# Kernel tuning notes

Measured on AMD Instinct MI355X. Metric: run time of the kernel, lower is better.

Reference implementation:

```python
import jax, jax.numpy as jnp
import numpy as np

B, L, D, H = 2, 1024, 1024, 16
HD = D // H  # 64


def _skew(x):
    # x: (BH, L, 2L-1) -> (BH, L, L); Music-Transformer skew trick.
    BH, Lx, _ = x.shape
    x = jnp.pad(x, ((0, 0), (0, 0), (1, 0)))            # (BH, L, 2L)
    x = x.reshape(BH, 2 * Lx * Lx)                        # flatten
    x = jnp.pad(x, ((0, 0), (0, Lx - 1)))                 # append L-1 zeros
    x = x.reshape(BH, Lx + 1, 2 * Lx - 1)
    return x[:, :Lx, Lx - 1:]


def setup_inputs() -> dict:
    key = jax.random.key(0)
    ks = jax.random.split(key, 10)
    s = 1.0 / np.sqrt(D)
    return {
        "x": jax.random.normal(ks[0], (B, L, D), jnp.float32),
        "Wq": jax.random.normal(ks[1], (D, D), jnp.float32) * s,
        "bq": jnp.zeros((D,), jnp.float32),
        "Wk": jax.random.normal(ks[2], (D, D), jnp.float32) * s,
        "bk": jnp.zeros((D,), jnp.float32),
        "Wv": jax.random.normal(ks[3], (D, D), jnp.float32) * s,
        "bv": jnp.zeros((D,), jnp.float32),
        "Wo": jax.random.normal(ks[4], (D, D), jnp.float32) * s,
        "bo": jnp.zeros((D,), jnp.float32),
        "rel_pos_emb": jax.random.normal(ks[5], (2 * L - 1, HD), jnp.float32),
    }


def reference(x, Wq, bq, Wk, bk, Wv, bv, Wo, bo, rel_pos_emb):
    Bx, Lx, Dx = x.shape
    hd = Dx // H
    scale = hd ** (-0.5)
    # projections (torch Linear: x @ W.T + b)
    q = (x @ Wq.T + bq).reshape(Bx, Lx, H, hd).transpose(0, 2, 1, 3)  # (B,H,L,hd)
    k = (x @ Wk.T + bk).reshape(Bx, Lx, H, hd).transpose(0, 2, 1, 3)
    v = (x @ Wv.T + bv).reshape(Bx, Lx, H, hd).transpose(0, 2, 1, 3)
    scores = jnp.einsum('bhid,bhjd->bhij', q, k)                      # (B,H,L,L)
    rel = jnp.einsum('bhid,rd->bhir', q, rel_pos_emb)                 # (B,H,L,2L-1)
    rel = _skew(rel.reshape(Bx * H, Lx, 2 * Lx - 1)).reshape(Bx, H, Lx, Lx)
    attn = jax.nn.softmax((scores + rel) * scale, axis=-1)
    ctx = jnp.einsum('bhij,bhjd->bhid', attn, v)                      # (B,H,L,hd)
    ctx = ctx.transpose(0, 2, 1, 3).reshape(Bx, Lx, Dx)
    return ctx @ Wo.T + bo
```

## Files before the change

### kernel.cpp

```cpp
#include <hip/hip_runtime.h>
#include <hip/hip_bf16.h>

typedef __bf16 bf16_t;
typedef __bf16 bf16x8 __attribute__((ext_vector_type(8)));
typedef __bf16 bf16x4 __attribute__((ext_vector_type(4)));
typedef float f32x4 __attribute__((ext_vector_type(4)));

#define B_ 2
#define L_ 1024
#define D_ 1024
#define H_ 16
#define HD_ 64

template <int CTRL>
static __device__ __forceinline__ float dpp_fmax(float v) {
    const int t = __builtin_amdgcn_update_dpp(0, __float_as_int(v), CTRL,
                                              0xF, 0xF, true);
    return fmaxf(v, __int_as_float(t));
}

__global__ __launch_bounds__(256) void prep_kernel(
    const float* __restrict__ x,
    const float* __restrict__ Wq, const float* __restrict__ Wk,
    const float* __restrict__ Wv, const float* __restrict__ Wo,
    const float* __restrict__ E,
    bf16_t* __restrict__ xb,
    bf16_t* __restrict__ Wqb, bf16_t* __restrict__ Wkb,
    bf16_t* __restrict__ Wvb, bf16_t* __restrict__ Wob,
    bf16_t* __restrict__ Eb) {
    const int bid = blockIdx.x;
    if (bid < 6144) {
        const float* src;
        bf16_t* dst;
        int i;
        if (bid < 2048) {
            src = x; dst = xb; i = bid * 256 + threadIdx.x;
        } else {
            const int z = (bid - 2048) >> 10;
            src = (z == 0) ? Wq : (z == 1) ? Wk : (z == 2) ? Wv : Wo;
            dst = (z == 0) ? Wqb : (z == 1) ? Wkb : (z == 2) ? Wvb : Wob;
            i = ((bid - 2048) & 1023) * 256 + threadIdx.x;
        }
        const float4 v = ((const float4*)src)[i];
        bf16x4 o;
        o[0] = (bf16_t)v.x; o[1] = (bf16_t)v.y;
        o[2] = (bf16_t)v.z; o[3] = (bf16_t)v.w;
        ((bf16x4*)dst)[i] = o;
    } else {
        const int idx = (bid - 6144) * 256 + threadIdx.x;
        if (idx < 64) Eb[idx] = (bf16_t)0.f;
        if (idx < 2047 * 64) Eb[64 + idx] = (bf16_t)E[idx];
    }
}

__global__ __launch_bounds__(256) void qkv_gemm_kernel(
    const bf16_t* __restrict__ xb,
    const bf16_t* __restrict__ Wqb, const bf16_t* __restrict__ Wkb,
    const bf16_t* __restrict__ Wvb,
    const float* __restrict__ bq, const float* __restrict__ bk2,
    const float* __restrict__ bv2,
    bf16_t* __restrict__ qbh, bf16_t* __restrict__ kbh,
    bf16_t* __restrict__ vtb) {
    constexpr int K = D_;
    __shared__ __align__(16) bf16_t As[64][72];
    __shared__ __align__(16) bf16_t Bs[64][72];

    const int z = blockIdx.z;
    const bf16_t* W = (z == 0) ? Wqb : (z == 1) ? Wkb : Wvb;
    const float* bias = (z == 0) ? bq : (z == 1) ? bk2 : bv2;
    const float alpha = (z == 0) ? 0.125f : 1.0f;

    const int tid = threadIdx.x;
    const int m0 = blockIdx.y * 64;
    const int n0 = blockIdx.x * 64;
    const int wave = tid >> 6;
    const int lane = tid & 63;
    const int wm = (wave >> 1) << 5;
    const int wn = (wave & 1) << 5;
    const int lrow = lane & 15;
    const int quad = lane >> 4;
    const int r0 = tid >> 3;
    const int c8 = (tid & 7) << 3;

    f32x4 acc[2][2] = {};

    uint4 pA0 = *(const uint4*)&xb[(size_t)(m0 + r0) * K + c8];
    uint4 pA1 = *(const uint4*)&xb[(size_t)(m0 + r0 + 32) * K + c8];
    uint4 pB0 = *(const uint4*)&W[(size_t)(n0 + r0) * K + c8];
    uint4 pB1 = *(const uint4*)&W[(size_t)(n0 + r0 + 32) * K + c8];

    for (int k0 = 0; k0 < K; k0 += 64) {
        *(uint4*)&As[r0][c8] = pA0;
        *(uint4*)&As[r0 + 32][c8] = pA1;
        *(uint4*)&Bs[r0][c8] = pB0;
        *(uint4*)&Bs[r0 + 32][c8] = pB1;
        const int kn = (k0 + 64 < K) ? k0 + 64 : k0;
        pA0 = *(const uint4*)&xb[(size_t)(m0 + r0) * K + kn + c8];
        pA1 = *(const uint4*)&xb[(size_t)(m0 + r0 + 32) * K + kn + c8];
        pB0 = *(const uint4*)&W[(size_t)(n0 + r0) * K + kn + c8];
        pB1 = *(const uint4*)&W[(size_t)(n0 + r0 + 32) * K + kn + c8];
        __syncthreads();

#pragma unroll
        for (int kc = 0; kc < 2; ++kc) {
            bf16x8 af[2], bfr[2];
            af[0]  = *(const bf16x8*)&As[wm + lrow][kc * 32 + 8 * quad];
            af[1]  = *(const bf16x8*)&As[wm + 16 + lrow][kc * 32 + 8 * quad];
            bfr[0] = *(const bf16x8*)&Bs[wn + lrow][kc * 32 + 8 * quad];
            bfr[1] = *(const bf16x8*)&Bs[wn + 16 + lrow][kc * 32 + 8 * quad];
#pragma unroll
            for (int t = 0; t < 2; ++t)
#pragma unroll
                for (int u = 0; u < 2; ++u)
                    acc[t][u] = __builtin_amdgcn_mfma_f32_16x16x32_bf16(
                        af[t], bfr[u], acc[t][u], 0, 0, 0);
        }
        __syncthreads();
    }

#pragma unroll
    for (int t = 0; t < 2; ++t) {
#pragma unroll
        for (int u = 0; u < 2; ++u) {
            const int col = n0 + wn + u * 16 + lrow;
            const float bvv = bias[col];
            const int h = col >> 6, d = col & 63;
            if (z < 2) {
                bf16_t* outp = z ? kbh : qbh;
#pragma unroll
                for (int r = 0; r < 4; ++r) {
                    const int row = m0 + wm + t * 16 + quad * 4 + r;
                    const int b = row >> 10, i = row & 1023;
                    outp[((size_t)((b * H_ + h) * L_ + i)) * HD_ + d] =
                        (bf16_t)((acc[t][u][r] + bvv) * alpha);
                }
            } else {
                const int row0 = m0 + wm + t * 16 + quad * 4;
                const int b = row0 >> 10, i = row0 & 1023;
                bf16x4 pk;
#pragma unroll
                for (int r = 0; r < 4; ++r) pk[r] = (bf16_t)(acc[t][u][r] + bvv);
                *(bf16x4*)&vtb[((size_t)((b * H_ + h) * HD_ + d)) * L_ + i] = pk;
            }
        }
    }
}

__global__ __launch_bounds__(256) void out_gemm_kernel(
    const bf16_t* __restrict__ A, const bf16_t* __restrict__ W,
    const float* __restrict__ bias, float* __restrict__ outF) {
    constexpr int K = D_;
    __shared__ __align__(16) bf16_t As[64][72];
    __shared__ __align__(16) bf16_t Bs[64][72];

    const int tid = threadIdx.x;
    const int m0 = blockIdx.y * 64;
    const int n0 = blockIdx.x * 64;
    const int wave = tid >> 6;
    const int lane = tid & 63;
    const int wm = (wave >> 1) << 5;
    const int wn = (wave & 1) << 5;
    const int lrow = lane & 15;
    const int quad = lane >> 4;
    const int r0 = tid >> 3;
    const int c8 = (tid & 7) << 3;

    f32x4 acc[2][2] = {};

    uint4 pA0 = *(const uint4*)&A[(size_t)(m0 + r0) * K + c8];
    uint4 pA1 = *(const uint4*)&A[(size_t)(m0 + r0 + 32) * K + c8];
    uint4 pB0 = *(const uint4*)&W[(size_t)(n0 + r0) * K + c8];
    uint4 pB1 = *(const uint4*)&W[(size_t)(n0 + r0 + 32) * K + c8];

    for (int k0 = 0; k0 < K; k0 += 64) {
        *(uint4*)&As[r0][c8] = pA0;
        *(uint4*)&As[r0 + 32][c8] = pA1;
        *(uint4*)&Bs[r0][c8] = pB0;
        *(uint4*)&Bs[r0 + 32][c8] = pB1;
        const int kn = (k0 + 64 < K) ? k0 + 64 : k0;
        pA0 = *(const uint4*)&A[(size_t)(m0 + r0) * K + kn + c8];
        pA1 = *(const uint4*)&A[(size_t)(m0 + r0 + 32) * K + kn + c8];
        pB0 = *(const uint4*)&W[(size_t)(n0 + r0) * K + kn + c8];
        pB1 = *(const uint4*)&W[(size_t)(n0 + r0 + 32) * K + kn + c8];
        __syncthreads();

#pragma unroll
        for (int kc = 0; kc < 2; ++kc) {
            bf16x8 af[2], bfr[2];
            af[0]  = *(const bf16x8*)&As[wm + lrow][kc * 32 + 8 * quad];
            af[1]  = *(const bf16x8*)&As[wm + 16 + lrow][kc * 32 + 8 * quad];
            bfr[0] = *(const bf16x8*)&Bs[wn + lrow][kc * 32 + 8 * quad];
            bfr[1] = *(const bf16x8*)&Bs[wn + 16 + lrow][kc * 32 + 8 * quad];
#pragma unroll
            for (int t = 0; t < 2; ++t)
#pragma unroll
                for (int u = 0; u < 2; ++u)
                    acc[t][u] = __builtin_amdgcn_mfma_f32_16x16x32_bf16(
                        af[t], bfr[u], acc[t][u], 0, 0, 0);
        }
        __syncthreads();
    }

#pragma unroll
    for (int t = 0; t < 2; ++t) {
#pragma unroll
        for (int u = 0; u < 2; ++u) {
            const int col = n0 + wn + u * 16 + lrow;
            const float bvv = bias[col];
#pragma unroll
            for (int r = 0; r < 4; ++r) {
                const int row = m0 + wm + t * 16 + quad * 4 + r;
                outF[(size_t)row * D_ + col] = acc[t][u][r] + bvv;
            }
        }
    }
}

__global__ __launch_bounds__(256) void fattn_kernel(
    const bf16_t* __restrict__ qbh, const bf16_t* __restrict__ kbh,
    const bf16_t* __restrict__ vtb, const bf16_t* __restrict__ Eb,
    bf16_t* __restrict__ ctx) {
    __shared__ __align__(16) char smem[33792];
    float (*Om)[32][64] = (float(*)[32][64])smem;
    float (*ml)[32][2]  = (float(*)[32][2])(smem + 32768);

    const int tid = threadIdx.x;
    const int w = tid >> 6;
    const int lane = tid & 63;
    const int q4 = lane >> 4;
    const int n = lane & 15;
    const int bh = blockIdx.y;
    const int b = bh >> 4;
    const int h = bh & 15;
    const int ib = blockIdx.x * 32;

    bf16_t* band = (bf16_t*)smem + (size_t)w * (96 * 40);
    bf16_t* ps = band;

    bf16x8 ones;
#pragma unroll
    for (int e = 0; e < 8; ++e) ones[e] = (bf16_t)1.0f;

    bf16x8 aq[2][2];
#pragma unroll
    for (int m = 0; m < 2; ++m) {
        const bf16x8* qrow =
            (const bf16x8*)(qbh + ((size_t)bh * L_ + ib + 16 * m + n) * HD_);
        aq[m][0] = qrow[q4];
        aq[m][1] = qrow[4 + q4];
    }

    const bf16_t* vbase = vtb + (size_t)bh * HD_ * L_;

    f32x4 o[2][4] = {};
    float m_r[2][4], l_r[2][4];
#pragma unroll
    for (int m = 0; m < 2; ++m)
#pragma unroll
        for (int r = 0; r < 4; ++r) { m_r[m][r] = -1e30f; l_r[m][r] = 0.f; }

    for (int t = 0; t < 4; ++t) {
        const int j0 = w * 256 + t * 64;

        bf16x8 bk[4][2];
#pragma unroll
        for (int u = 0; u < 4; ++u)
#pragma unroll
            for (int kc = 0; kc < 2; ++kc)
                bk[u][kc] = *(const bf16x8*)(kbh +
                    ((size_t)bh * L_ + j0 + 16 * u + n) * HD_ + kc * 32 + 8 * q4);

        const int rbase = j0 - ib + 992;
#pragma unroll
        for (int up = 0; up < 6; ++up) {
            f32x4 rc[2] = {};
#pragma unroll
            for (int kc = 0; kc < 2; ++kc) {
                const bf16x8 be = *(const bf16x8*)(Eb +
                    ((size_t)(rbase + 16 * up + n)) * HD_ + kc * 32 + 8 * q4);
#pragma unroll
                for (int m = 0; m < 2; ++m)
                    rc[m] = __builtin_amdgcn_mfma_f32_16x16x32_bf16(
                        aq[m][kc], be, rc[m], 0, 0, 0);
            }
#pragma unroll
            for (int m = 0; m < 2; ++m) {
                bf16x4 pk;
#pragma unroll
                for (int r = 0; r < 4; ++r) pk[r] = (bf16_t)rc[m][r];
                *(bf16x4*)&band[(size_t)(16 * up + n) * 40 + 16 * m + 4 * q4] = pk;
            }
        }

        f32x4 s[2][4] = {};
#pragma unroll
        for (int u = 0; u < 4; ++u)
#pragma unroll
            for (int kc = 0; kc < 2; ++kc)
#pragma unroll
                for (int m = 0; m < 2; ++m)
                    s[m][u] = __builtin_amdgcn_mfma_f32_16x16x32_bf16(
                        aq[m][kc], bk[u][kc], s[m][u], 0, 0, 0);

        bf16x8 vf[4][2];
#pragma unroll
        for (int u = 0; u < 4; ++u)
#pragma unroll
            for (int kc = 0; kc < 2; ++kc)
                vf[u][kc] = *(const bf16x8*)(vbase +
                    ((size_t)(16 * u + n)) * L_ + j0 + kc * 32 + 8 * q4);

#pragma unroll
        for (int m = 0; m < 2; ++m)
#pragma unroll
            for (int u = 0; u < 4; ++u)
#pragma unroll
                for (int r = 0; r < 4; ++r) {
                    const int row = 16 * m + 4 * q4 + r;
                    s[m][u][r] +=
                        (float)band[(size_t)(16 * u + n - row + 31) * 40 + row];
                }

        float al[2][4];
#pragma unroll
        for (int m = 0; m < 2; ++m) {
#pragma unroll
            for (int r = 0; r < 4; ++r) {
                float mt = fmaxf(fmaxf(s[m][0][r], s[m][1][r]),
                                 fmaxf(s[m][2][r], s[m][3][r]));
                mt = dpp_fmax<0x121>(mt);
                mt = dpp_fmax<0x122>(mt);
                mt = dpp_fmax<0x124>(mt);
                mt = dpp_fmax<0x128>(mt);
                const float mn = fmaxf(m_r[m][r], mt);
                al[m][r] = __expf(m_r[m][r] - mn);
                m_r[m][r] = mn;
#pragma unroll
                for (int u = 0; u < 4; ++u) {
                    s[m][u][r] = __expf(s[m][u][r] - mn);
                    o[m][u][r] *= al[m][r];
                }
            }
        }

#pragma unroll
        for (int m = 0; m < 2; ++m)
#pragma unroll
            for (int u = 0; u < 4; ++u)
#pragma unroll
                for (int r = 0; r < 4; ++r)
                    ps[(size_t)(16 * m + 4 * q4 + r) * 72 + 16 * u + n] =
                        (bf16_t)s[m][u][r];

        bf16x8 pa[2][2];
#pragma unroll
        for (int m = 0; m < 2; ++m) {
            pa[m][0] = *(const bf16x8*)&ps[(size_t)(16 * m + n) * 72 + 8 * q4];
            pa[m][1] = *(const bf16x8*)&ps[(size_t)(16 * m + n) * 72 + 32 + 8 * q4];
        }

#pragma unroll
        for (int m = 0; m < 2; ++m) {
            f32x4 z = {};
            z = __builtin_amdgcn_mfma_f32_16x16x32_bf16(pa[m][0], ones, z, 0, 0, 0);
            z = __builtin_amdgcn_mfma_f32_16x16x32_bf16(pa[m][1], ones, z, 0, 0, 0);
#pragma unroll
            for (int r = 0; r < 4; ++r)
                l_r[m][r] = l_r[m][r] * al[m][r] + z[r];
        }

#pragma unroll
        for (int u = 0; u < 4; ++u)
#pragma unroll
            for (int kc = 0; kc < 2; ++kc)
#pragma unroll
                for (int m = 0; m < 2; ++m)
                    o[m][u] = __builtin_amdgcn_mfma_f32_16x16x32_bf16(
                        pa[m][kc], vf[u][kc], o[m][u], 0, 0, 0);
    }

    __syncthreads();
#pragma unroll
    for (int m = 0; m < 2; ++m)
#pragma unroll
        for (int u = 0; u < 4; ++u)
#pragma unroll
            for (int r = 0; r < 4; ++r)
                Om[w][16 * m + 4 * q4 + r][16 * u + n] = o[m][u][r];
    if (n == 0) {
#pragma unroll
        for (int m = 0; m < 2; ++m)
#pragma unroll
            for (int r = 0; r < 4; ++r) {
                ml[w][16 * m + 4 * q4 + r][0] = m_r[m][r];
                ml[w][16 * m + 4 * q4 + r][1] = l_r[m][r];
            }
    }
    __syncthreads();

    {
        const int row = tid >> 3;
        const int c0 = (tid & 7) * 8;
        const float m0v = ml[0][row][0], m1v = ml[1][row][0];
        const float m2v = ml[2][row][0], m3v = ml[3][row][0];
        const float ms = fmaxf(fmaxf(m0v, m1v), fmaxf(m2v, m3v));
        const float a0 = __expf(m0v - ms), a1 = __expf(m1v - ms);
        const float a2 = __expf(m2v - ms), a3 = __expf(m3v - ms);
        const float inv = 1.f / (a0 * ml[0][row][1] + a1 * ml[1][row][1] +
                                 a2 * ml[2][row][1] + a3 * ml[3][row][1]);
        bf16_t* dst = ctx + ((size_t)(b * L_ + ib + row)) * D_ + h * HD_ + c0;
#pragma unroll
        for (int cc = 0; cc < 8; ++cc) {
            const int col = c0 + cc;
            const float val = (a0 * Om[0][row][col] + a1 * Om[1][row][col] +
                               a2 * Om[2][row][col] + a3 * Om[3][row][col]) * inv;
            dst[cc] = (bf16_t)val;
        }
    }
}

extern "C" void kernel_launch(void* const* d_in, const int* in_sizes, int n_in,
                              void* d_out, int out_size, void* d_ws,
                              size_t ws_size, hipStream_t stream) {
    const float* x   = (const float*)d_in[0];
    const float* Wq  = (const float*)d_in[1];
    const float* bq  = (const float*)d_in[2];
    const float* Wk  = (const float*)d_in[3];
    const float* bk  = (const float*)d_in[4];
    const float* Wv  = (const float*)d_in[5];
    const float* bv  = (const float*)d_in[6];
    const float* Wo  = (const float*)d_in[7];
    const float* bo  = (const float*)d_in[8];
    const float* E   = (const float*)d_in[9];
    float* out = (float*)d_out;

    char* ws = (char*)d_ws;
    const size_t MB = 1024u * 1024u;
    bf16_t* xb   = (bf16_t*)(ws);
    bf16_t* Wqb  = (bf16_t*)(ws + 4 * MB);
    bf16_t* Wkb  = (bf16_t*)(ws + 6 * MB);
    bf16_t* Wvb  = (bf16_t*)(ws + 8 * MB);
    bf16_t* Wob  = (bf16_t*)(ws + 10 * MB);
    bf16_t* qbh  = (bf16_t*)(ws + 12 * MB);
    bf16_t* kbh  = (bf16_t*)(ws + 16 * MB);
    bf16_t* vtb  = (bf16_t*)(ws + 20 * MB);
    bf16_t* ctxb = (bf16_t*)(ws + 24 * MB);
    bf16_t* Eb   = (bf16_t*)(ws + 28 * MB);

    prep_kernel<<<6656, 256, 0, stream>>>(x, Wq, Wk, Wv, Wo, E,
                                          xb, Wqb, Wkb, Wvb, Wob, Eb);

    dim3 gq(D_ / 64, (B_ * L_) / 64, 3);
    qkv_gemm_kernel<<<gq, 256, 0, stream>>>(xb, Wqb, Wkb, Wvb, bq, bk, bv,
                                            qbh, kbh, vtb);

    dim3 ga(L_ / 32, B_ * H_);
    fattn_kernel<<<ga, 256, 0, stream>>>(qbh, kbh, vtb, Eb, ctxb);

    dim3 gg(D_ / 64, (B_ * L_) / 64);
    out_gemm_kernel<<<gg, 256, 0, stream>>>(ctxb, Wob, bo, out);
}
```

Before: 185.0 us.

## Halve attention query tile to 16 rows, use exp2 softmax, vectorize ctx store

The attention kernel now handles 16 query rows per block instead of 32, doubling the grid to 64x32 blocks, shrinking shared memory, and adding a launch-bounds occupancy hint of 5. The q scale folds in log2(e) so softmax can use the native exp2 instruction instead of __expf. The final context write packs four bf16 values into one vector store, and the Om buffer is padded to 65 columns to avoid bank conflicts. Smaller tiles mean K/V/E fragments are reloaded twice as often per query row, which trades data reuse for occupancy and parallelism.

Measured after the change: 237.9 us. +28.6%, slower.

```diff
diff --git a/kernel.cpp b/kernel.cpp
--- a/kernel.cpp
+++ b/kernel.cpp
@@ -68,7 +68,7 @@
     const int z = blockIdx.z;
     const bf16_t* W = (z == 0) ? Wqb : (z == 1) ? Wkb : Wvb;
     const float* bias = (z == 0) ? bq : (z == 1) ? bk2 : bv2;
-    const float alpha = (z == 0) ? 0.125f : 1.0f;
+    const float alpha = (z == 0) ? 0.18033688011112043f : 1.0f;
 
     const int tid = threadIdx.x;
     const int m0 = blockIdx.y * 64;
@@ -216,13 +216,13 @@
     }
 }
 
-__global__ __launch_bounds__(256) void fattn_kernel(
+__global__ __launch_bounds__(256, 5) void fattn_kernel(
     const bf16_t* __restrict__ qbh, const bf16_t* __restrict__ kbh,
     const bf16_t* __restrict__ vtb, const bf16_t* __restrict__ Eb,
     bf16_t* __restrict__ ctx) {
-    __shared__ __align__(16) char smem[33792];
-    float (*Om)[32][64] = (float(*)[32][64])smem;
-    float (*ml)[32][2]  = (float(*)[32][2])(smem + 32768);
+    __shared__ __align__(16) char smem[25600];
+    float (*Om)[16][65] = (float(*)[16][65])smem;
+    float (*ml)[16][2]  = (float(*)[16][2])(smem + 16640);
 
     const int tid = threadIdx.x;
     const int w = tid >> 6;
@@ -232,32 +232,29 @@
     const int bh = blockIdx.y;
     const int b = bh >> 4;
     const int h = bh & 15;
-    const int ib = blockIdx.x * 32;
-
-    bf16_t* band = (bf16_t*)smem + (size_t)w * (96 * 40);
+    const int ib = blockIdx.x * 16;
+
+    bf16_t* band = (bf16_t*)smem + (size_t)w * (80 * 40);
     bf16_t* ps = band;
 
     bf16x8 ones;
 #pragma unroll
     for (int e = 0; e < 8; ++e) ones[e] = (bf16_t)1.0f;
 
-    bf16x8 aq[2][2];
-#pragma unroll
-    for (int m = 0; m < 2; ++m) {
+    bf16x8 aq[2];
+    {
         const bf16x8* qrow =
-            (const bf16x8*)(qbh + ((size_t)bh * L_ + ib + 16 * m + n) * HD_);
-        aq[m][0] = qrow[q4];
-        aq[m][1] = qrow[4 + q4];
+            (const bf16x8*)(qbh + ((size_t)bh * L_ + ib + n) * HD_);
+        aq[0] = qrow[q4];
+        aq[1] = qrow[4 + q4];
     }
 
     const bf16_t* vbase = vtb + (size_t)bh * HD_ * L_;
 
-    f32x4 o[2][4] = {};
-    float m_r[2][4], l_r[2][4];
-#pragma unroll
-    for (int m = 0; m < 2; ++m)
-#pragma unroll
-        for (int r = 0; r < 4; ++r) { m_r[m][r] = -1e30f; l_r[m][r] = 0.f; }
+    f32x4 o[4] = {};
+    float m_r[4], l_r[4];
+#pragma unroll
+    for (int r = 0; r < 4; ++r) { m_r[r] = -1e30f; l_r[r] = 0.f; }
 
     for (int t = 0; t < 4; ++t) {
         const int j0 = w * 256 + t * 64;
@@ -270,37 +267,30 @@
                 bk[u][kc] = *(const bf16x8*)(kbh +
                     ((size_t)bh * L_ + j0 + 16 * u + n) * HD_ + kc * 32 + 8 * q4);
 
-        const int rbase = j0 - ib + 992;
-#pragma unroll
-        for (int up = 0; up < 6; ++up) {
-            f32x4 rc[2] = {};
+        const int rbase = j0 - ib + 1008;
+#pragma unroll
+        for (int up = 0; up < 5; ++up) {
+            f32x4 rc = {};
 #pragma unroll
             for (int kc = 0; kc < 2; ++kc) {
                 const bf16x8 be = *(const bf16x8*)(Eb +
                     ((size_t)(rbase + 16 * up + n)) * HD_ + kc * 32 + 8 * q4);
-#pragma unroll
-                for (int m = 0; m < 2; ++m)
-                    rc[m] = __builtin_amdgcn_mfma_f32_16x16x32_bf16(
-                        aq[m][kc], be, rc[m], 0, 0, 0);
+                rc = __builtin_amdgcn_mfma_f32_16x16x32_bf16(
+                    aq[kc], be, rc, 0, 0, 0);
             }
-#pragma unroll
-            for (int m = 0; m < 2; ++m) {
-                bf16x4 pk;
-#pragma unroll
-                for (int r = 0; r < 4; ++r) pk[r] = (bf16_t)rc[m][r];
-                *(bf16x4*)&band[(size_t)(16 * up + n) * 40 + 16 * m + 4 * q4] = pk;
-            }
-        }
-
-        f32x4 s[2][4] = {};
+            bf16x4 pk;
+#pragma unroll
+            for (int r = 0; r < 4; ++r) pk[r] = (bf16_t)rc[r];
+            *(bf16x4*)&band[(size_t)(16 * up + n) * 40 + 4 * q4] = pk;
+        }
+
+        f32x4 s[4] = {};
 #pragma unroll
         for (int u = 0; u < 4; ++u)
 #pragma unroll
             for (int kc = 0; kc < 2; ++kc)
-#pragma unroll
-                for (int m = 0; m < 2; ++m)
-                    s[m][u] = __builtin_amdgcn_mfma_f32_16x16x32_bf16(
-                        aq[m][kc], bk[u][kc], s[m][u], 0, 0, 0);
+                s[u] = __builtin_amdgcn_mfma_f32_16x16x32_bf16(
+                    aq[kc], bk[u][kc], s[u], 0, 0, 0);
 
         bf16x8 vf[4][2];
 #pragma unroll
@@ -311,111 +301,97 @@
                     ((size_t)(16 * u + n)) * L_ + j0 + kc * 32 + 8 * q4);
 
 #pragma unroll
-        for (int m = 0; m < 2; ++m)
-#pragma unroll
-            for (int u = 0; u < 4; ++u)
-#pragma unroll
-                for (int r = 0; r < 4; ++r) {
-                    const int row = 16 * m + 4 * q4 + r;
-                    s[m][u][r] +=
-                        (float)band[(size_t)(16 * u + n - row + 31) * 40 + row];
-                }
-
-        float al[2][4];
-#pragma unroll
-        for (int m = 0; m < 2; ++m) {
+        for (int u = 0; u < 4; ++u)
 #pragma unroll
             for (int r = 0; r < 4; ++r) {
-                float mt = fmaxf(fmaxf(s[m][0][r], s[m][1][r]),
-                                 fmaxf(s[m][2][r], s[m][3][r]));
-                mt = dpp_fmax<0x121>(mt);
-                mt = dpp_fmax<0x122>(mt);
-                mt = dpp_fmax<0x124>(mt);
-                mt = dpp_fmax<0x128>(mt);
-                const float mn = fmaxf(m_r[m][r], mt);
-                al[m][r] = __expf(m_r[m][r] - mn);
-                m_r[m][r] = mn;
-#pragma unroll
-                for (int u = 0; u < 4; ++u) {
-                    s[m][u][r] = __expf(s[m][u][r] - mn);
-                    o[m][u][r] *= al[m][r];
-                }
+                const int row = 4 * q4 + r;
+                s[u][r] +=
+                    (float)band[(size_t)(16 * u + n - row + 15) * 40 + row];
             }
-        }
-
-#pragma unroll
-        for (int m = 0; m < 2; ++m)
-#pragma unroll
-            for (int u = 0; u < 4; ++u)
-#pragma unroll
-                for (int r = 0; r < 4; ++r)
-                    ps[(size_t)(16 * m + 4 * q4 + r) * 72 + 16 * u + n] =
-                        (bf16_t)s[m][u][r];
-
-        bf16x8 pa[2][2];
-#pragma unroll
-        for (int m = 0; m < 2; ++m) {
-            pa[m][0] = *(const bf16x8*)&ps[(size_t)(16 * m + n) * 72 + 8 * q4];
-            pa[m][1] = *(const bf16x8*)&ps[(size_t)(16 * m + n) * 72 + 32 + 8 * q4];
-        }
-
-#pragma unroll
-        for (int m = 0; m < 2; ++m) {
+
+        float al[4];
+#pragma unroll
+        for (int r = 0; r < 4; ++r) {
+            float mt = fmaxf(fmaxf(s[0][r], s[1][r]),
+                             fmaxf(s[2][r], s[3][r]));
+            mt = dpp_fmax<0x121>(mt);
+            mt = dpp_fmax<0x122>(mt);
+            mt = dpp_fmax<0x124>(mt);
+            mt = dpp_fmax<0x128>(mt);
+            const float mn = fmaxf(m_r[r], mt);
+            al[r] = __builtin_amdgcn_exp2f(m_r[r] - mn);
+            m_r[r] = mn;
+#pragma unroll
+            for (int u = 0; u < 4; ++u) {
+                s[u][r] = __builtin_amdgcn_exp2f(s[u][r] - mn);
+                o[u][r] *= al[r];
+            }
+        }
+
+#pragma unroll
+        for (int u = 0; u < 4; ++u)
+#pragma unroll
+            for (int r = 0; r < 4; ++r)
+                ps[(size_t)(4 * q4 + r) * 72 + 16 * u + n] = (bf16_t)s[u][r];
+
+        bf16x8 pa[2];
+        pa[0] = *(const bf16x8*)&ps[(size_t)n * 72 + 8 * q4];
+        pa[1] = *(const bf16x8*)&ps[(size_t)n * 72 + 32 + 8 * q4];
+
+        {
             f32x4 z = {};
-            z = __builtin_amdgcn_mfma_f32_16x16x32_bf16(pa[m][0], ones, z, 0, 0, 0);
-            z = __builtin_amdgcn_mfma_f32_16x16x32_bf16(pa[m][1], ones, z, 0, 0, 0);
+            z = __builtin_amdgcn_mfma_f32_16x16x32_bf16(pa[0], ones, z, 0, 0, 0);
+            z = __builtin_amdgcn_mfma_f32_16x16x32_bf16(pa[1], ones, z, 0, 0, 0);
 #pragma unroll
             for (int r = 0; r < 4; ++r)
-                l_r[m][r] = l_r[m][r] * al[m][r] + z[r];
+                l_r[r] = l_r[r] * al[r] + z[r];
         }
 
 #pragma unroll
         for (int u = 0; u < 4; ++u)
 #pragma unroll
             for (int kc = 0; kc < 2; ++kc)
-#pragma unroll
-                for (int m = 0; m < 2; ++m)
-                    o[m][u] = __builtin_amdgcn_mfma_f32_16x16x32_bf16(
-                        pa[m][kc], vf[u][kc], o[m][u], 0, 0, 0);
+                o[u] = __builtin_amdgcn_mfma_f32_16x16x32_bf16(
+                    pa[kc], vf[u][kc], o[u], 0, 0, 0);
     }
 
     __syncthreads();
 #pragma unroll
-    for (int m = 0; m < 2; ++m)
-#pragma unroll
-        for (int u = 0; u < 4; ++u)
-#pragma unroll
-            for (int r = 0; r < 4; ++r)
-                Om[w][16 * m + 4 * q4 + r][16 * u + n] = o[m][u][r];
+    for (int u = 0; u < 4; ++u)
+#pragma unroll
+        for (int r = 0; r < 4; ++r)
+            Om[w][4 * q4 + r][16 * u + n] = o[u][r];
     if (n == 0) {
 #pragma unroll
-        for (int m = 0; m < 2; ++m)
-#pragma unroll
-            for (int r = 0; r < 4; ++r) {
-                ml[w][16 * m + 4 * q4 + r][0] = m_r[m][r];
-                ml[w][16 * m + 4 * q4 + r][1] = l_r[m][r];
-            }
+        for (int r = 0; r < 4; ++r) {
+            ml[w][4 * q4 + r][0] = m_r[r];
+            ml[w][4 * q4 + r][1] = l_r[r];
+        }
     }
     __syncthreads();
 
     {
-        const int row = tid >> 3;
-        const int c0 = (tid & 7) * 8;
+        const int row = tid >> 4;
+        const int c0 = (tid & 15) * 4;
         const float m0v = ml[0][row][0], m1v = ml[1][row][0];
         const float m2v = ml[2][row][0], m3v = ml[3][row][0];
         const float ms = fmaxf(fmaxf(m0v, m1v), fmaxf(m2v, m3v));
-        const float a0 = __expf(m0v - ms), a1 = __expf(m1v - ms);
-        const float a2 = __expf(m2v - ms), a3 = __expf(m3v - ms);
+        const float a0 = __builtin_amdgcn_exp2f(m0v - ms);
+        const float a1 = __builtin_amdgcn_exp2f(m1v - ms);
+        const float a2 = __builtin_amdgcn_exp2f(m2v - ms);
+        const float a3 = __builtin_amdgcn_exp2f(m3v - ms);
         const float inv = 1.f / (a0 * ml[0][row][1] + a1 * ml[1][row][1] +
                                  a2 * ml[2][row][1] + a3 * ml[3][row][1]);
         bf16_t* dst = ctx + ((size_t)(b * L_ + ib + row)) * D_ + h * HD_ + c0;
-#pragma unroll
-        for (int cc = 0; cc < 8; ++cc) {
+        bf16x4 pk;
+#pragma unroll
+        for (int cc = 0; cc < 4; ++cc) {
             const int col = c0 + cc;
             const float val = (a0 * Om[0][row][col] + a1 * Om[1][row][col] +
                                a2 * Om[2][row][col] + a3 * Om[3][row][col]) * inv;
-            dst[cc] = (bf16_t)val;
-        }
+            pk[cc] = (bf16_t)val;
+        }
+        *(bf16x4*)dst = pk;
     }
 }
 
@@ -454,7 +430,7 @@
     qkv_gemm_kernel<<<gq, 256, 0, stream>>>(xb, Wqb, Wkb, Wvb, bq, bk, bv,
                                             qbh, kbh, vtb);
 
-    dim3 ga(L_ / 32, B_ * H_);
+    dim3 ga(L_ / 16, B_ * H_);
     fattn_kernel<<<ga, 256, 0, stream>>>(qbh, kbh, vtb, Eb, ctxb);
 
     dim3 gg(D_ / 64, (B_ * L_) / 64);
```

## Use 128x128 GEMM tiles with direct global-to-LDS loads and exp2 softmax

Applied to the files above, without the earlier changes.

Both projection GEMMs move from 64x64 to 128x128 block tiles, with each wave computing a 64x64 sub-tile. They now fill shared memory with global_load_lds direct-to-LDS transfers instead of register prefetch followed by LDS stores. The attention softmax switches from __expf to the hardware exp2 instruction, with log2(e) folded into the Q scaling constant. This cuts global traffic per FLOP and exp overhead, but the grids become small (128 blocks for the output GEMM). The unpadded LDS rows may also cause bank conflicts, and the prefetch overlap between loads and MFMA is lost.

New measurement: 198.2 us. 7.1% more time.

```diff
diff --git a/kernel.cpp b/kernel.cpp
--- a/kernel.cpp
+++ b/kernel.cpp
@@ -11,6 +11,9 @@
 #define D_ 1024
 #define H_ 16
 #define HD_ 64
+
+#define AS1 __attribute__((address_space(1)))
+#define AS3 __attribute__((address_space(3)))
 
 template <int CTRL>
 static __device__ __forceinline__ float dpp_fmax(float v) {
@@ -62,56 +65,57 @@
     bf16_t* __restrict__ qbh, bf16_t* __restrict__ kbh,
     bf16_t* __restrict__ vtb) {
     constexpr int K = D_;
-    __shared__ __align__(16) bf16_t As[64][72];
-    __shared__ __align__(16) bf16_t Bs[64][72];
+    __shared__ __align__(16) bf16_t As[128 * 64];
+    __shared__ __align__(16) bf16_t Bs[128 * 64];
 
     const int z = blockIdx.z;
     const bf16_t* W = (z == 0) ? Wqb : (z == 1) ? Wkb : Wvb;
     const float* bias = (z == 0) ? bq : (z == 1) ? bk2 : bv2;
-    const float alpha = (z == 0) ? 0.125f : 1.0f;
+    const float alpha = (z == 0) ? 0.18033688011112043f : 1.0f;
 
     const int tid = threadIdx.x;
-    const int m0 = blockIdx.y * 64;
-    const int n0 = blockIdx.x * 64;
-    const int wave = tid >> 6;
+    const int w = tid >> 6;
     const int lane = tid & 63;
-    const int wm = (wave >> 1) << 5;
-    const int wn = (wave & 1) << 5;
-    const int lrow = lane & 15;
-    const int quad = lane >> 4;
-    const int r0 = tid >> 3;
-    const int c8 = (tid & 7) << 3;
-
-    f32x4 acc[2][2] = {};
-
-    uint4 pA0 = *(const uint4*)&xb[(size_t)(m0 + r0) * K + c8];
-    uint4 pA1 = *(const uint4*)&xb[(size_t)(m0 + r0 + 32) * K + c8];
-    uint4 pB0 = *(const uint4*)&W[(size_t)(n0 + r0) * K + c8];
-    uint4 pB1 = *(const uint4*)&W[(size_t)(n0 + r0 + 32) * K + c8];
+    const int n = lane & 15;
+    const int q4 = lane >> 4;
+    const int wr = w >> 1;
+    const int wc = w & 1;
+    const int m0 = blockIdx.y * 128;
+    const int n0 = blockIdx.x * 128;
+
+    const int sr = (lane >> 3);
+    const int sc = (lane & 7) * 8;
+
+    f32x4 acc[4][4] = {};
 
     for (int k0 = 0; k0 < K; k0 += 64) {
-        *(uint4*)&As[r0][c8] = pA0;
-        *(uint4*)&As[r0 + 32][c8] = pA1;
-        *(uint4*)&Bs[r0][c8] = pB0;
-        *(uint4*)&Bs[r0 + 32][c8] = pB1;
-        const int kn = (k0 + 64 < K) ? k0 + 64 : k0;
-        pA0 = *(const uint4*)&xb[(size_t)(m0 + r0) * K + kn + c8];
-        pA1 = *(const uint4*)&xb[(size_t)(m0 + r0 + 32) * K + kn + c8];
-        pB0 = *(const uint4*)&W[(size_t)(n0 + r0) * K + kn + c8];
-        pB1 = *(const uint4*)&W[(size_t)(n0 + r0 + 32) * K + kn + c8];
+#pragma unroll
+        for (int i = 0; i < 4; ++i) {
+            const int row = w * 32 + i * 8;
+            __builtin_amdgcn_global_load_lds(
+                (const AS1 void*)&xb[(size_t)(m0 + row + sr) * K + k0 + sc],
+                (AS3 void*)&As[row * 64], 16, 0, 0);
+            __builtin_amdgcn_global_load_lds(
+                (const AS1 void*)&W[(size_t)(n0 + row + sr) * K + k0 + sc],
+                (AS3 void*)&Bs[row * 64], 16, 0, 0);
+        }
         __syncthreads();
 
 #pragma unroll
         for (int kc = 0; kc < 2; ++kc) {
-            bf16x8 af[2], bfr[2];
-            af[0]  = *(const bf16x8*)&As[wm + lrow][kc * 32 + 8 * quad];
-            af[1]  = *(const bf16x8*)&As[wm + 16 + lrow][kc * 32 + 8 * quad];
-            bfr[0] = *(const bf16x8*)&Bs[wn + lrow][kc * 32 + 8 * quad];
-            bfr[1] = *(const bf16x8*)&Bs[wn + 16 + lrow][kc * 32 + 8 * quad];
-#pragma unroll
-            for (int t = 0; t < 2; ++t)
-#pragma unroll
-                for (int u = 0; u < 2; ++u)
+            bf16x8 af[4], bfr[4];
+#pragma unroll
+            for (int t = 0; t < 4; ++t)
+                af[t] = *(const bf16x8*)&As[(wr * 64 + t * 16 + n) * 64 +
+                                            kc * 32 + 8 * q4];
+#pragma unroll
+            for (int u = 0; u < 4; ++u)
+                bfr[u] = *(const bf16x8*)&Bs[(wc * 64 + u * 16 + n) * 64 +
+                                             kc * 32 + 8 * q4];
+#pragma unroll
+            for (int t = 0; t < 4; ++t)
+#pragma unroll
+                for (int u = 0; u < 4; ++u)
                     acc[t][u] = __builtin_amdgcn_mfma_f32_16x16x32_bf16(
                         af[t], bfr[u], acc[t][u], 0, 0, 0);
         }
@@ -119,23 +123,23 @@
     }
 
 #pragma unroll
-    for (int t = 0; t < 2; ++t) {
-#pragma unroll
-        for (int u = 0; u < 2; ++u) {
-            const int col = n0 + wn + u * 16 + lrow;
+    for (int t = 0; t < 4; ++t) {
+#pragma unroll
+        for (int u = 0; u < 4; ++u) {
+            const int col = n0 + wc * 64 + u * 16 + n;
             const float bvv = bias[col];
             const int h = col >> 6, d = col & 63;
             if (z < 2) {
                 bf16_t* outp = z ? kbh : qbh;
 #pragma unroll
                 for (int r = 0; r < 4; ++r) {
-                    const int row = m0 + wm + t * 16 + quad * 4 + r;
+                    const int row = m0 + wr * 64 + t * 16 + q4 * 4 + r;
                     const int b = row >> 10, i = row & 1023;
                     outp[((size_t)((b * H_ + h) * L_ + i)) * HD_ + d] =
                         (bf16_t)((acc[t][u][r] + bvv) * alpha);
                 }
             } else {
-                const int row0 = m0 + wm + t * 16 + quad * 4;
+                const int row0 = m0 + wr * 64 + t * 16 + q4 * 4;
                 const int b = row0 >> 10, i = row0 & 1023;
                 bf16x4 pk;
 #pragma unroll
@@ -150,51 +154,52 @@
     const bf16_t* __restrict__ A, const bf16_t* __restrict__ W,
     const float* __restrict__ bias, float* __restrict__ outF) {
     constexpr int K = D_;
-    __shared__ __align__(16) bf16_t As[64][72];
-    __shared__ __align__(16) bf16_t Bs[64][72];
+    __shared__ __align__(16) bf16_t As[128 * 64];
+    __shared__ __align__(16) bf16_t Bs[128 * 64];
 
     const int tid = threadIdx.x;
-    const int m0 = blockIdx.y * 64;
-    const int n0 = blockIdx.x * 64;
-    const int wave = tid >> 6;
+    const int w = tid >> 6;
     const int lane = tid & 63;
-    const int wm = (wave >> 1) << 5;
-    const int wn = (wave & 1) << 5;
-    const int lrow = lane & 15;
-    const int quad = lane >> 4;
-    const int r0 = tid >> 3;
-    const int c8 = (tid & 7) << 3;
-
-    f32x4 acc[2][2] = {};
-
-    uint4 pA0 = *(const uint4*)&A[(size_t)(m0 + r0) * K + c8];
-    uint4 pA1 = *(const uint4*)&A[(size_t)(m0 + r0 + 32) * K + c8];
-    uint4 pB0 = *(const uint4*)&W[(size_t)(n0 + r0) * K + c8];
-    uint4 pB1 = *(const uint4*)&W[(size_t)(n0 + r0 + 32) * K + c8];
+    const int n = lane & 15;
+    const int q4 = lane >> 4;
+    const int wr = w >> 1;
+    const int wc = w & 1;
+    const int m0 = blockIdx.y * 128;
+    const int n0 = blockIdx.x * 128;
+
+    const int sr = (lane >> 3);
+    const int sc = (lane & 7) * 8;
+
+    f32x4 acc[4][4] = {};
 
     for (int k0 = 0; k0 < K; k0 += 64) {
-        *(uint4*)&As[r0][c8] = pA0;
-        *(uint4*)&As[r0 + 32][c8] = pA1;
-        *(uint4*)&Bs[r0][c8] = pB0;
-        *(uint4*)&Bs[r0 + 32][c8] = pB1;
-        const int kn = (k0 + 64 < K) ? k0 + 64 : k0;
-        pA0 = *(const uint4*)&A[(size_t)(m0 + r0) * K + kn + c8];
-        pA1 = *(const uint4*)&A[(size_t)(m0 + r0 + 32) * K + kn + c8];
-        pB0 = *(const uint4*)&W[(size_t)(n0 + r0) * K + kn + c8];
-        pB1 = *(const uint4*)&W[(size_t)(n0 + r0 + 32) * K + kn + c8];
+#pragma unroll
+        for (int i = 0; i < 4; ++i) {
+            const int row = w * 32 + i * 8;
+            __builtin_amdgcn_global_load_lds(
+                (const AS1 void*)&A[(size_t)(m0 + row + sr) * K + k0 + sc],
+                (AS3 void*)&As[row * 64], 16, 0, 0);
+            __builtin_amdgcn_global_load_lds(
+                (const AS1 void*)&W[(size_t)(n0 + row + sr) * K + k0 + sc],
+                (AS3 void*)&Bs[row * 64], 16, 0, 0);
+        }
         __syncthreads();
 
 #pragma unroll
         for (int kc = 0; kc < 2; ++kc) {
-            bf16x8 af[2], bfr[2];
-            af[0]  = *(const bf16x8*)&As[wm + lrow][kc * 32 + 8 * quad];
-            af[1]  = *(const bf16x8*)&As[wm + 16 + lrow][kc * 32 + 8 * quad];
-            bfr[0] = *(const bf16x8*)&Bs[wn + lrow][kc * 32 + 8 * quad];
-            bfr[1] = *(const bf16x8*)&Bs[wn + 16 + lrow][kc * 32 + 8 * quad];
-#pragma unroll
-            for (int t = 0; t < 2; ++t)
-#pragma unroll
-                for (int u = 0; u < 2; ++u)
+            bf16x8 af[4], bfr[4];
+#pragma unroll
+            for (int t = 0; t < 4; ++t)
+                af[t] = *(const bf16x8*)&As[(wr * 64 + t * 16 + n) * 64 +
+                                            kc * 32 + 8 * q4];
+#pragma unroll
+            for (int u = 0; u < 4; ++u)
+                bfr[u] = *(const bf16x8*)&Bs[(wc * 64 + u * 16 + n) * 64 +
+                                             kc * 32 + 8 * q4];
+#pragma unroll
+            for (int t = 0; t < 4; ++t)
+#pragma unroll
+                for (int u = 0; u < 4; ++u)
                     acc[t][u] = __builtin_amdgcn_mfma_f32_16x16x32_bf16(
                         af[t], bfr[u], acc[t][u], 0, 0, 0);
         }
@@ -202,14 +207,14 @@
     }
 
 #pragma unroll
-    for (int t = 0; t < 2; ++t) {
-#pragma unroll
-        for (int u = 0; u < 2; ++u) {
-            const int col = n0 + wn + u * 16 + lrow;
+    for (int t = 0; t < 4; ++t) {
+#pragma unroll
+        for (int u = 0; u < 4; ++u) {
+            const int col = n0 + wc * 64 + u * 16 + n;
             const float bvv = bias[col];
 #pragma unroll
             for (int r = 0; r < 4; ++r) {
-                const int row = m0 + wm + t * 16 + quad * 4 + r;
+                const int row = m0 + wr * 64 + t * 16 + q4 * 4 + r;
                 outF[(size_t)row * D_ + col] = acc[t][u][r] + bvv;
             }
         }
@@ -333,11 +338,11 @@
                 mt = dpp_fmax<0x124>(mt);
                 mt = dpp_fmax<0x128>(mt);
                 const float mn = fmaxf(m_r[m][r], mt);
-                al[m][r] = __expf(m_r[m][r] - mn);
+                al[m][r] = __builtin_amdgcn_exp2f(m_r[m][r] - mn);
                 m_r[m][r] = mn;
 #pragma unroll
                 for (int u = 0; u < 4; ++u) {
-                    s[m][u][r] = __expf(s[m][u][r] - mn);
+                    s[m][u][r] = __builtin_amdgcn_exp2f(s[m][u][r] - mn);
                     o[m][u][r] *= al[m][r];
                 }
             }
@@ -404,8 +409,10 @@
         const float m0v = ml[0][row][0], m1v = ml[1][row][0];
         const float m2v = ml[2][row][0], m3v = ml[3][row][0];
         const float ms = fmaxf(fmaxf(m0v, m1v), fmaxf(m2v, m3v));
-        const float a0 = __expf(m0v - ms), a1 = __expf(m1v - ms);
-        const float a2 = __expf(m2v - ms), a3 = __expf(m3v - ms);
+        const float a0 = __builtin_amdgcn_exp2f(m0v - ms);
+        const float a1 = __builtin_amdgcn_exp2f(m1v - ms);
+        const float a2 = __builtin_amdgcn_exp2f(m2v - ms);
+        const float a3 = __builtin_amdgcn_exp2f(m3v - ms);
         const float inv = 1.f / (a0 * ml[0][row][1] + a1 * ml[1][row][1] +
                                  a2 * ml[2][row][1] + a3 * ml[3][row][1]);
         bf16_t* dst = ctx + ((size_t)(b * L_ + ib + row)) * D_ + h * HD_ + c0;
@@ -450,13 +457,13 @@
     prep_kernel<<<6656, 256, 0, stream>>>(x, Wq, Wk, Wv, Wo, E,
                                           xb, Wqb, Wkb, Wvb, Wob, Eb);
 
-    dim3 gq(D_ / 64, (B_ * L_) / 64, 3);
+    dim3 gq(D_ / 128, (B_ * L_) / 128, 3);
     qkv_gemm_kernel<<<gq, 256, 0, stream>>>(xb, Wqb, Wkb, Wvb, bq, bk, bv,
                                             qbh, kbh, vtb);
 
     dim3 ga(L_ / 32, B_ * H_);
     fattn_kernel<<<ga, 256, 0, stream>>>(qbh, kbh, vtb, Eb, ctxb);
 
-    dim3 gg(D_ / 64, (B_ * L_) / 64);
+    dim3 gg(D_ / 128, (B_ * L_) / 128);
     out_gemm_kernel<<<gg, 256, 0, stream>>>(ctxb, Wob, bo, out);
 }
```

## Fuse weight fp32-to-bf16 conversion into GEMM loads and use exp2 softmax

Applied to the files above, without the earlier changes.

Drops the separate bf16 conversion pass over the four weight matrices. The QKV and output GEMMs now load fp32 weights directly and convert them to bf16 while staging into shared memory. This removes one prep pass and its workspace round trip, at the cost of doubled weight bytes read per tile, and each weight tile is re-read by many blocks. Separately, the query scale now folds in log2(e), so the softmax can use the native exp2 instruction instead of __expf.

Result: no change. 186.9 us (+1.0%).

```diff
diff --git a/kernel.cpp b/kernel.cpp
--- a/kernel.cpp
+++ b/kernel.cpp
@@ -19,35 +19,28 @@
     return fmaxf(v, __int_as_float(t));
 }
 
+static __device__ __forceinline__ bf16x8 cvt8(const float4 a, const float4 b) {
+    bf16x8 o;
+    o[0] = (bf16_t)a.x; o[1] = (bf16_t)a.y;
+    o[2] = (bf16_t)a.z; o[3] = (bf16_t)a.w;
+    o[4] = (bf16_t)b.x; o[5] = (bf16_t)b.y;
+    o[6] = (bf16_t)b.z; o[7] = (bf16_t)b.w;
+    return o;
+}
+
 __global__ __launch_bounds__(256) void prep_kernel(
-    const float* __restrict__ x,
-    const float* __restrict__ Wq, const float* __restrict__ Wk,
-    const float* __restrict__ Wv, const float* __restrict__ Wo,
-    const float* __restrict__ E,
-    bf16_t* __restrict__ xb,
-    bf16_t* __restrict__ Wqb, bf16_t* __restrict__ Wkb,
-    bf16_t* __restrict__ Wvb, bf16_t* __restrict__ Wob,
-    bf16_t* __restrict__ Eb) {
+    const float* __restrict__ x, const float* __restrict__ E,
+    bf16_t* __restrict__ xb, bf16_t* __restrict__ Eb) {
     const int bid = blockIdx.x;
-    if (bid < 6144) {
-        const float* src;
-        bf16_t* dst;
-        int i;
-        if (bid < 2048) {
-            src = x; dst = xb; i = bid * 256 + threadIdx.x;
-        } else {
-            const int z = (bid - 2048) >> 10;
-            src = (z == 0) ? Wq : (z == 1) ? Wk : (z == 2) ? Wv : Wo;
-            dst = (z == 0) ? Wqb : (z == 1) ? Wkb : (z == 2) ? Wvb : Wob;
-            i = ((bid - 2048) & 1023) * 256 + threadIdx.x;
-        }
-        const float4 v = ((const float4*)src)[i];
+    if (bid < 2048) {
+        const int i = bid * 256 + threadIdx.x;
+        const float4 v = ((const float4*)x)[i];
         bf16x4 o;
         o[0] = (bf16_t)v.x; o[1] = (bf16_t)v.y;
         o[2] = (bf16_t)v.z; o[3] = (bf16_t)v.w;
-        ((bf16x4*)dst)[i] = o;
+        ((bf16x4*)xb)[i] = o;
     } else {
-        const int idx = (bid - 6144) * 256 + threadIdx.x;
+        const int idx = (bid - 2048) * 256 + threadIdx.x;
         if (idx < 64) Eb[idx] = (bf16_t)0.f;
         if (idx < 2047 * 64) Eb[64 + idx] = (bf16_t)E[idx];
     }
@@ -55,8 +48,8 @@
 
 __global__ __launch_bounds__(256) void qkv_gemm_kernel(
     const bf16_t* __restrict__ xb,
-    const bf16_t* __restrict__ Wqb, const bf16_t* __restrict__ Wkb,
-    const bf16_t* __restrict__ Wvb,
+    const float* __restrict__ Wqf, const float* __restrict__ Wkf,
+    const float* __restrict__ Wvf,
     const float* __restrict__ bq, const float* __restrict__ bk2,
     const float* __restrict__ bv2,
     bf16_t* __restrict__ qbh, bf16_t* __restrict__ kbh,
@@ -66,9 +59,9 @@
     __shared__ __align__(16) bf16_t Bs[64][72];
 
     const int z = blockIdx.z;
-    const bf16_t* W = (z == 0) ? Wqb : (z == 1) ? Wkb : Wvb;
+    const float* Wf = (z == 0) ? Wqf : (z == 1) ? Wkf : Wvf;
     const float* bias = (z == 0) ? bq : (z == 1) ? bk2 : bv2;
-    const float alpha = (z == 0) ? 0.125f : 1.0f;
+    const float alpha = (z == 0) ? 0.18033688011112043f : 1.0f;
 
     const int tid = threadIdx.x;
     const int m0 = blockIdx.y * 64;
@@ -86,19 +79,23 @@
 
     uint4 pA0 = *(const uint4*)&xb[(size_t)(m0 + r0) * K + c8];
     uint4 pA1 = *(const uint4*)&xb[(size_t)(m0 + r0 + 32) * K + c8];
-    uint4 pB0 = *(const uint4*)&W[(size_t)(n0 + r0) * K + c8];
-    uint4 pB1 = *(const uint4*)&W[(size_t)(n0 + r0 + 32) * K + c8];
+    float4 pB0a = *(const float4*)&Wf[(size_t)(n0 + r0) * K + c8];
+    float4 pB0b = *(const float4*)&Wf[(size_t)(n0 + r0) * K + c8 + 4];
+    float4 pB1a = *(const float4*)&Wf[(size_t)(n0 + r0 + 32) * K + c8];
+    float4 pB1b = *(const float4*)&Wf[(size_t)(n0 + r0 + 32) * K + c8 + 4];
 
     for (int k0 = 0; k0 < K; k0 += 64) {
         *(uint4*)&As[r0][c8] = pA0;
         *(uint4*)&As[r0 + 32][c8] = pA1;
-        *(uint4*)&Bs[r0][c8] = pB0;
-        *(uint4*)&Bs[r0 + 32][c8] = pB1;
+        *(bf16x8*)&Bs[r0][c8] = cvt8(pB0a, pB0b);
+        *(bf16x8*)&Bs[r0 + 32][c8] = cvt8(pB1a, pB1b);
         const int kn = (k0 + 64 < K) ? k0 + 64 : k0;
         pA0 = *(const uint4*)&xb[(size_t)(m0 + r0) * K + kn + c8];
         pA1 = *(const uint4*)&xb[(size_t)(m0 + r0 + 32) * K + kn + c8];
-        pB0 = *(const uint4*)&W[(size_t)(n0 + r0) * K + kn + c8];
-        pB1 = *(const uint4*)&W[(size_t)(n0 + r0 + 32) * K + kn + c8];
+        pB0a = *(const float4*)&Wf[(size_t)(n0 + r0) * K + kn + c8];
+        pB0b = *(const float4*)&Wf[(size_t)(n0 + r0) * K + kn + c8 + 4];
+        pB1a = *(const float4*)&Wf[(size_t)(n0 + r0 + 32) * K + kn + c8];
+        pB1b = *(const float4*)&Wf[(size_t)(n0 + r0 + 32) * K + kn + c8 + 4];
         __syncthreads();
 
 #pragma unroll
@@ -147,7 +144,7 @@
 }
 
 __global__ __launch_bounds__(256) void out_gemm_kernel(
-    const bf16_t* __restrict__ A, const bf16_t* __restrict__ W,
+    const bf16_t* __restrict__ A, const float* __restrict__ Wf,
     const float* __restrict__ bias, float* __restrict__ outF) {
     constexpr int K = D_;
     __shared__ __align__(16) bf16_t As[64][72];
@@ -169,19 +166,23 @@
 
     uint4 pA0 = *(const uint4*)&A[(size_t)(m0 + r0) * K + c8];
     uint4 pA1 = *(const uint4*)&A[(size_t)(m0 + r0 + 32) * K + c8];
-    uint4 pB0 = *(const uint4*)&W[(size_t)(n0 + r0) * K + c8];
-    uint4 pB1 = *(const uint4*)&W[(size_t)(n0 + r0 + 32) * K + c8];
+    float4 pB0a = *(const float4*)&Wf[(size_t)(n0 + r0) * K + c8];
+    float4 pB0b = *(const float4*)&Wf[(size_t)(n0 + r0) * K + c8 + 4];
+    float4 pB1a = *(const float4*)&Wf[(size_t)(n0 + r0 + 32) * K + c8];
+    float4 pB1b = *(const float4*)&Wf[(size_t)(n0 + r0 + 32) * K + c8 + 4];
 
     for (int k0 = 0; k0 < K; k0 += 64) {
         *(uint4*)&As[r0][c8] = pA0;
         *(uint4*)&As[r0 + 32][c8] = pA1;
-        *(uint4*)&Bs[r0][c8] = pB0;
-        *(uint4*)&Bs[r0 + 32][c8] = pB1;
+        *(bf16x8*)&Bs[r0][c8] = cvt8(pB0a, pB0b);
+        *(bf16x8*)&Bs[r0 + 32][c8] = cvt8(pB1a, pB1b);
         const int kn = (k0 + 64 < K) ? k0 + 64 : k0;
         pA0 = *(const uint4*)&A[(size_t)(m0 + r0) * K + kn + c8];
         pA1 = *(const uint4*)&A[(size_t)(m0 + r0 + 32) * K + kn + c8];
-        pB0 = *(const uint4*)&W[(size_t)(n0 + r0) * K + kn + c8];
-        pB1 = *(const uint4*)&W[(size_t)(n0 + r0 + 32) * K + kn + c8];
+        pB0a = *(const float4*)&Wf[(size_t)(n0 + r0) * K + kn + c8];
+        pB0b = *(const float4*)&Wf[(size_t)(n0 + r0) * K + kn + c8 + 4];
+        pB1a = *(const float4*)&Wf[(size_t)(n0 + r0 + 32) * K + kn + c8];
+        pB1b = *(const float4*)&Wf[(size_t)(n0 + r0 + 32) * K + kn + c8 + 4];
         __syncthreads();
 
 #pragma unroll
@@ -333,11 +334,11 @@
                 mt = dpp_fmax<0x124>(mt);
                 mt = dpp_fmax<0x128>(mt);
                 const float mn = fmaxf(m_r[m][r], mt);
-                al[m][r] = __expf(m_r[m][r] - mn);
+                al[m][r] = __builtin_amdgcn_exp2f(m_r[m][r] - mn);
                 m_r[m][r] = mn;
 #pragma unroll
                 for (int u = 0; u < 4; ++u) {
-                    s[m][u][r] = __expf(s[m][u][r] - mn);
+                    s[m][u][r] = __builtin_amdgcn_exp2f(s[m][u][r] - mn);
                     o[m][u][r] *= al[m][r];
                 }
             }
@@ -404,8 +405,10 @@
         const float m0v = ml[0][row][0], m1v = ml[1][row][0];
         const float m2v = ml[2][row][0], m3v = ml[3][row][0];
         const float ms = fmaxf(fmaxf(m0v, m1v), fmaxf(m2v, m3v));
-        const float a0 = __expf(m0v - ms), a1 = __expf(m1v - ms);
-        const float a2 = __expf(m2v - ms), a3 = __expf(m3v - ms);
+        const float a0 = __builtin_amdgcn_exp2f(m0v - ms);
+        const float a1 = __builtin_amdgcn_exp2f(m1v - ms);
+        const float a2 = __builtin_amdgcn_exp2f(m2v - ms);
+        const float a3 = __builtin_amdgcn_exp2f(m3v - ms);
         const float inv = 1.f / (a0 * ml[0][row][1] + a1 * ml[1][row][1] +
                                  a2 * ml[2][row][1] + a3 * ml[3][row][1]);
         bf16_t* dst = ctx + ((size_t)(b * L_ + ib + row)) * D_ + h * HD_ + c0;
@@ -437,26 +440,21 @@
     char* ws = (char*)d_ws;
     const size_t MB = 1024u * 1024u;
     bf16_t* xb   = (bf16_t*)(ws);
-    bf16_t* Wqb  = (bf16_t*)(ws + 4 * MB);
-    bf16_t* Wkb  = (bf16_t*)(ws + 6 * MB);
-    bf16_t* Wvb  = (bf16_t*)(ws + 8 * MB);
-    bf16_t* Wob  = (bf16_t*)(ws + 10 * MB);
-    bf16_t* qbh  = (bf16_t*)(ws + 12 * MB);
-    bf16_t* kbh  = (bf16_t*)(ws + 16 * MB);
-    bf16_t* vtb  = (bf16_t*)(ws + 20 * MB);
-    bf16_t* ctxb = (bf16_t*)(ws + 24 * MB);
-    bf16_t* Eb   = (bf16_t*)(ws + 28 * MB);
-
-    prep_kernel<<<6656, 256, 0, stream>>>(x, Wq, Wk, Wv, Wo, E,
-                                          xb, Wqb, Wkb, Wvb, Wob, Eb);
+    bf16_t* qbh  = (bf16_t*)(ws + 4 * MB);
+    bf16_t* kbh  = (bf16_t*)(ws + 8 * MB);
+    bf16_t* vtb  = (bf16_t*)(ws + 12 * MB);
+    bf16_t* ctxb = (bf16_t*)(ws + 16 * MB);
+    bf16_t* Eb   = (bf16_t*)(ws + 20 * MB);
+
+    prep_kernel<<<2560, 256, 0, stream>>>(x, E, xb, Eb);
 
     dim3 gq(D_ / 64, (B_ * L_) / 64, 3);
-    qkv_gemm_kernel<<<gq, 256, 0, stream>>>(xb, Wqb, Wkb, Wvb, bq, bk, bv,
+    qkv_gemm_kernel<<<gq, 256, 0, stream>>>(xb, Wq, Wk, Wv, bq, bk, bv,
                                             qbh, kbh, vtb);
 
     dim3 ga(L_ / 32, B_ * H_);
     fattn_kernel<<<ga, 256, 0, stream>>>(qbh, kbh, vtb, Eb, ctxb);
 
     dim3 gg(D_ / 64, (B_ * L_) / 64);
-    out_gemm_kernel<<<gg, 256, 0, stream>>>(ctxb, Wob, bo, out);
-}
+    out_gemm_kernel<<<gg, 256, 0, stream>>>(ctxb, Wo, bo, out);
+}
```
